# Optimization experiments

Measured on AMD Instinct MI355X. Metric: run time of the kernel, lower is better.

The kernel has to match this reference:

```python
import jax, jax.numpy as jnp
import numpy as np

REGION = 70  # region_width == region_height == receptive_field


def _localize(score_map, img_h, score_h):
    # stride=1, window=1x1 -> region_score is just the channel-mean at each pixel.
    B, _, Hs, Ws = score_map.shape
    m = score_map.mean(axis=1).reshape(B, -1)  # [B, Hs*Ws], row-major over (dim2, dim3)
    # loop order (i outer over dim2, j inner over dim3) + strict-inequality updates
    # == first-occurrence argmax/argmin in row-major order.
    imax = jnp.argmax(m, axis=1)
    vmax = jnp.max(m, axis=1)
    imin = jnp.argmin(m, axis=1)
    vmin = jnp.min(m, axis=1)
    rx = (imax // Ws).astype(jnp.float32)
    ry = (imax % Ws).astype(jnp.float32)
    fx = (imin // Ws).astype(jnp.float32)
    fy = (imin % Ws).astype(jnp.float32)
    # ax_tmp_real initialized to zeros (update iff score > 0); ax_tmp_fake to ones (iff score < 1)
    ax_real = jnp.where(vmax[:, None] > 0.0, jnp.stack([rx, ry], axis=1), 0.0)
    ax_fake = jnp.where(vmin[:, None] < 1.0, jnp.stack([fx, fy], axis=1), 1.0)
    img_stride = float((img_h - 70.0) // score_h)  # static python floor-div as in torch
    ax_real = ax_real * img_stride + 70.0
    ax_fake = ax_fake * img_stride + 70.0
    return ax_fake, ax_real


def _crop_one(img, row0, col0):
    # Faithful crop_and_resize (transform_fpcoor=True, crop size == box size == 70):
    # sample positions are row0 + [0..69], col0 + [0..69]; bilinear; zeros outside image.
    C, H, W = img.shape
    ys = row0 + jnp.arange(REGION, dtype=jnp.float32)
    xs = col0 + jnp.arange(REGION, dtype=jnp.float32)
    vy = (ys >= 0.0) & (ys <= H - 1.0)
    vx = (xs >= 0.0) & (xs <= W - 1.0)
    y0 = jnp.floor(ys)
    x0 = jnp.floor(xs)
    ly = ys - y0
    lx = xs - x0
    y0i = jnp.clip(y0.astype(jnp.int32), 0, H - 1)
    y1i = jnp.clip(y0i + 1, 0, H - 1)
    x0i = jnp.clip(x0.astype(jnp.int32), 0, W - 1)
    x1i = jnp.clip(x0i + 1, 0, W - 1)

    def gat(yi, xi):  # -> [C, 70, 70]
        return img[:, yi[:, None], xi[None, :]]

    top = gat(y0i, x0i) * (1.0 - lx)[None, None, :] + gat(y0i, x1i) * lx[None, None, :]
    bot = gat(y1i, x0i) * (1.0 - lx)[None, None, :] + gat(y1i, x1i) * lx[None, None, :]
    out = top * (1.0 - ly)[None, :, None] + bot * ly[None, :, None]
    mask = (vy[:, None] & vx[None, :]).astype(img.dtype)
    return out * mask[None]


_crop = jax.vmap(_crop_one)  # over batch


def _forward(real_B, fake_B, real_A, score_map):
    ax_fake, ax_real = _localize(score_map, real_B.shape[2], score_map.shape[2])
    ax_fake = jax.lax.stop_gradient(ax_fake)  # torch detaches via .cpu().numpy()
    ax_real = jax.lax.stop_gradient(ax_real)
    # boxes = [y, x, y+70, x+70] fed to RoIAlign as (x1,y1,x2,y2):
    # crop row start = ax[:,0] (the loop's _x, dim-2 index), col start = ax[:,1].
    fake_Bf = _crop(fake_B, ax_fake[:, 0], ax_fake[:, 1])
    real_Af = _crop(real_A, ax_fake[:, 0], ax_fake[:, 1])
    fake_ABf = jnp.concatenate((real_Af, fake_Bf), axis=1)
    fake_Br = _crop(fake_B, ax_real[:, 0], ax_real[:, 1])
    real_Ar = _crop(real_A, ax_real[:, 0], ax_real[:, 1])
    real_ABr = jnp.concatenate((real_Ar, fake_Br), axis=1)
    return (fake_Br, real_Ar, fake_Bf, real_Af, fake_ABf, real_ABr)


def setup_inputs() -> dict:
    key = jax.random.key(0)
    k1, k2, k3, k4 = jax.random.split(key, 4)
    B, H = 32, 512
    return {
        "real_B": jax.random.normal(k1, (B, 3, H, H), dtype=jnp.float32),
        "fake_B": jax.random.normal(k2, (B, 3, H, H), dtype=jnp.float32),
        "real_A": jax.random.normal(k3, (B, 3, H, H), dtype=jnp.float32),
        "score_map": jax.random.uniform(k4, (B, 1, 128, 128), dtype=jnp.float32),
    }


def reference(real_B, fake_B, real_A, score_map):
    return _forward(real_B, fake_B, real_A, score_map)
```

## Files before the change

kernel.cpp:

```cpp
#include <hip/hip_runtime.h>

#define SSZ   16384
#define SW    128
#define IMG   512
#define NPER  470400
#define OFF_AB_F 1881600
#define OFF_AB_R 2822400
#define CHUNKS 32
#define NF4_BATCH 14700
#define F4_PER_CHUNK 460

typedef float f4v __attribute__((ext_vector_type(4)));

__global__ __launch_bounds__(256)
void fused_crop_kernel(const float* __restrict__ fake_B,
                       const float* __restrict__ real_A,
                       const float* __restrict__ score,
                       float* __restrict__ out) {
    const int blk   = blockIdx.x;
    const int b     = blk >> 5;
    const int chunk = blk & 31;
    const int t     = threadIdx.x;

    const float4* s4 = (const float4*)(score + (size_t)b * SSZ);
    float vmax = -__builtin_inff(); int imax = 0;
    float vmin =  __builtin_inff(); int imin = 0;
    #pragma unroll
    for (int it = 0; it < 16; ++it) {
        const int q = it * 256 + t;
        const float4 v = s4[q];
        const int e = q * 4;
        if (v.x > vmax) { vmax = v.x; imax = e;     }
        if (v.y > vmax) { vmax = v.y; imax = e + 1; }
        if (v.z > vmax) { vmax = v.z; imax = e + 2; }
        if (v.w > vmax) { vmax = v.w; imax = e + 3; }
        if (v.x < vmin) { vmin = v.x; imin = e;     }
        if (v.y < vmin) { vmin = v.y; imin = e + 1; }
        if (v.z < vmin) { vmin = v.z; imin = e + 2; }
        if (v.w < vmin) { vmin = v.w; imin = e + 3; }
    }
    #pragma unroll
    for (int off = 1; off < 64; off <<= 1) {
        const float mv = __shfl_xor(vmax, off); const int mi = __shfl_xor(imax, off);
        if (mv > vmax || (mv == vmax && mi < imax)) { vmax = mv; imax = mi; }
        const float nv = __shfl_xor(vmin, off); const int ni = __shfl_xor(imin, off);
        if (nv < vmin || (nv == vmin && ni < imin)) { vmin = nv; imin = ni; }
    }
    __shared__ float sv[8];
    __shared__ int   si[8];
    if ((t & 63) == 0) {
        const int w = t >> 6;
        sv[w] = vmax; si[w] = imax;
        sv[w + 4] = vmin; si[w + 4] = imin;
    }
    __syncthreads();
    float bmax = sv[0]; int bimax = si[0];
    float bmin = sv[4]; int bimin = si[4];
    #pragma unroll
    for (int w = 1; w < 4; ++w) {
        if (sv[w] > bmax || (sv[w] == bmax && si[w] < bimax)) { bmax = sv[w]; bimax = si[w]; }
        if (sv[w+4] < bmin || (sv[w+4] == bmin && si[w+4] < bimin)) { bmin = sv[w+4]; bimin = si[w+4]; }
    }
    int rr, rc, fr, fc;
    if (bmax > 0.0f) { rr = bimax / SW; rc = bimax % SW; } else { rr = 0; rc = 0; }
    if (bmin < 1.0f) { fr = bimin / SW; fc = bimin % SW; } else { fr = 1; fc = 1; }
    const int row0r = rr * 3 + 70, col0r = rc * 3 + 70;
    const int row0f = fr * 3 + 70, col0f = fc * 3 + 70;

    const size_t srcb = (size_t)b * 3 * (IMG * IMG);
    const int e0 = chunk * F4_PER_CHUNK;
    const int e1 = min(e0 + F4_PER_CHUNK, NF4_BATCH);
    for (int e = e0 + t; e < e1; e += 256) {
        const int k    = e / 3675;
        const int rem  = e - k * 3675;
        const int c    = rem / 1225;
        const int f4   = rem - c * 1225;
        const int flat = f4 * 4;
        const int i0   = flat / 70;
        const int j0   = flat - i0 * 70;

        const int row0 = (k < 2) ? row0r : row0f;
        const int col0 = (k < 2) ? col0r : col0f;
        const float* src = (k == 0 || k == 2) ? fake_B : real_A;
        const float* sp  = src + srcb + (size_t)c * (IMG * IMG);

        f4v v;
        #pragma unroll
        for (int s = 0; s < 4; ++s) {
            int i = i0, j = j0 + s;
            if (j >= 70) { j -= 70; ++i; }
            const int y = row0 + i, x = col0 + j;
            v[s] = (y < IMG && x < IMG) ? sp[y * IMG + x] : 0.0f;
        }

        const size_t inner = (size_t)c * 4900 + flat;
        const size_t prim  = (size_t)k * NPER + (size_t)b * 14700 + inner;
        const size_t cb    = ((k < 2) ? (size_t)OFF_AB_R : (size_t)OFF_AB_F)
                             + (size_t)b * 29400
                             + ((k & 1) ? 0 : 3) * 4900
                             + inner;
        __builtin_nontemporal_store(v, (f4v*)(out + prim));
        __builtin_nontemporal_store(v, (f4v*)(out + cb));
    }
}

extern "C" void kernel_launch(void* const* d_in, const int* in_sizes, int n_in,
                              void* d_out, int out_size, void* d_ws, size_t ws_size,
                              hipStream_t stream) {
    const float* fake_B    = (const float*)d_in[1];
    const float* real_A    = (const float*)d_in[2];
    const float* score_map = (const float*)d_in[3];
    float* out = (float*)d_out;

    fused_crop_kernel<<<32 * CHUNKS, 256, 0, stream>>>(fake_B, real_A, score_map, out);
}
```

Before: 18.11 us.

## Split localization into separate partial-reduction kernel and double crop chunk count

Before, each of the 32 crop blocks per batch re-read the whole 64KB score map to find argmax/argmin. Now a small kernel reduces 16 slices per batch into packed sortable 64-bit keys in workspace. The crop kernel merges those 32 keys and runs on twice as many smaller chunks. This removes the redundant score reads, but adds a second kernel launch and a dependency between the two kernels.

```diff
diff --git a/kernel.cpp b/kernel.cpp
--- a/kernel.cpp
+++ b/kernel.cpp
@@ -6,30 +6,31 @@
 #define NPER  470400
 #define OFF_AB_F 1881600
 #define OFF_AB_R 2822400
-#define CHUNKS 32
 #define NF4_BATCH 14700
-#define F4_PER_CHUNK 460
+#define CHUNKS 64
+#define F4_PER_CHUNK 230
 
 typedef float f4v __attribute__((ext_vector_type(4)));
+typedef unsigned long long u64;
 
-__global__ __launch_bounds__(256)
-void fused_crop_kernel(const float* __restrict__ fake_B,
-                       const float* __restrict__ real_A,
-                       const float* __restrict__ score,
-                       float* __restrict__ out) {
-    const int blk   = blockIdx.x;
-    const int b     = blk >> 5;
-    const int chunk = blk & 31;
-    const int t     = threadIdx.x;
+__device__ __forceinline__ unsigned ord_f32(float v) {
+    unsigned s = __float_as_uint(v);
+    return (s & 0x80000000u) ? ~s : (s | 0x80000000u);
+}
 
-    const float4* s4 = (const float4*)(score + (size_t)b * SSZ);
+__global__ __launch_bounds__(64)
+void localize_partial(const float* __restrict__ score, u64* __restrict__ keys) {
+    const int blk = blockIdx.x;
+    const int b = blk >> 4, sl = blk & 15;
+    const int t = threadIdx.x;
+    const float4* p4 = (const float4*)(score + (size_t)b * SSZ + sl * 1024);
+
     float vmax = -__builtin_inff(); int imax = 0;
     float vmin =  __builtin_inff(); int imin = 0;
     #pragma unroll
-    for (int it = 0; it < 16; ++it) {
-        const int q = it * 256 + t;
-        const float4 v = s4[q];
-        const int e = q * 4;
+    for (int q = 0; q < 4; ++q) {
+        const float4 v = p4[t + 64 * q];
+        const int e = sl * 1024 + (t + 64 * q) * 4;
         if (v.x > vmax) { vmax = v.x; imax = e;     }
         if (v.y > vmax) { vmax = v.y; imax = e + 1; }
         if (v.z > vmax) { vmax = v.z; imax = e + 2; }
@@ -46,21 +47,36 @@
         const float nv = __shfl_xor(vmin, off); const int ni = __shfl_xor(imin, off);
         if (nv < vmin || (nv == vmin && ni < imin)) { vmin = nv; imin = ni; }
     }
-    __shared__ float sv[8];
-    __shared__ int   si[8];
-    if ((t & 63) == 0) {
-        const int w = t >> 6;
-        sv[w] = vmax; si[w] = imax;
-        sv[w + 4] = vmin; si[w + 4] = imin;
+    if (t == 0) {
+        keys[b * 32 + sl]      = ((u64)ord_f32(vmax) << 32) | (unsigned)~imax;
+        keys[b * 32 + 16 + sl] = ((u64)ord_f32(vmin) << 32) | (unsigned)imin;
     }
-    __syncthreads();
-    float bmax = sv[0]; int bimax = si[0];
-    float bmin = sv[4]; int bimin = si[4];
+}
+
+__global__ __launch_bounds__(256)
+void crop_kernel(const float* __restrict__ fake_B,
+                 const float* __restrict__ real_A,
+                 const u64* __restrict__ keys,
+                 float* __restrict__ out) {
+    const int blk   = blockIdx.x;
+    const int b     = blk / CHUNKS;
+    const int chunk = blk % CHUNKS;
+    const int t     = threadIdx.x;
+
+    const u64* kb = keys + b * 32;
+    u64 km = kb[0], kn = kb[16];
     #pragma unroll
-    for (int w = 1; w < 4; ++w) {
-        if (sv[w] > bmax || (sv[w] == bmax && si[w] < bimax)) { bmax = sv[w]; bimax = si[w]; }
-        if (sv[w+4] < bmin || (sv[w+4] == bmin && si[w+4] < bimin)) { bmin = sv[w+4]; bimin = si[w+4]; }
+    for (int s = 1; s < 16; ++s) {
+        const u64 a = kb[s];      if (a > km) km = a;
+        const u64 c = kb[16 + s]; if (c < kn) kn = c;
     }
+    const unsigned uh = (unsigned)(km >> 32);
+    const float bmax = __uint_as_float((uh & 0x80000000u) ? (uh & 0x7FFFFFFFu) : ~uh);
+    const int bimax = (int)~(unsigned)km;
+    const unsigned un = (unsigned)(kn >> 32);
+    const float bmin = __uint_as_float((un & 0x80000000u) ? (un & 0x7FFFFFFFu) : ~un);
+    const int bimin = (int)(unsigned)kn;
+
     int rr, rc, fr, fc;
     if (bmax > 0.0f) { rr = bimax / SW; rc = bimax % SW; } else { rr = 0; rc = 0; }
     if (bmin < 1.0f) { fr = bimin / SW; fc = bimin % SW; } else { fr = 1; fc = 1; }
@@ -81,9 +97,8 @@
 
         const int row0 = (k < 2) ? row0r : row0f;
         const int col0 = (k < 2) ? col0r : col0f;
-        const float* src = (k == 0 || k == 2) ? fake_B : real_A;
-        const float* sp  = src + srcb + (size_t)c * (IMG * IMG);
-
+        const float* sp = ((k == 0 || k == 2) ? fake_B : real_A)
+                          + srcb + (size_t)c * (IMG * IMG);
         f4v v;
         #pragma unroll
         for (int s = 0; s < 4; ++s) {
@@ -111,6 +126,8 @@
     const float* real_A    = (const float*)d_in[2];
     const float* score_map = (const float*)d_in[3];
     float* out = (float*)d_out;
+    u64*   keys = (u64*)d_ws;
 
-    fused_crop_kernel<<<32 * CHUNKS, 256, 0, stream>>>(fake_B, real_A, score_map, out);
+    localize_partial<<<32 * 16, 64, 0, stream>>>(score_map, keys);
+    crop_kernel<<<32 * CHUNKS, 256, 0, stream>>>(fake_B, real_A, keys, out);
 }
```

After: 15.93 us. -12.1%, faster.

## Use fewer larger blocks, vectorized unaligned row loads, and plain stores

Applied to the files above, without the earlier changes.

Changes the launch from 1024 blocks of 256 threads to 256 blocks of 1024 threads, so each batch's score argmax/argmin is recomputed 8 times instead of 32. The gather now uses a single unaligned 4-wide load when the four elements lie in one row and inside the image, and falls back to scalar loads otherwise. Nontemporal output stores are replaced with ordinary vector stores. The trade-off is fewer blocks across the CUs (256 blocks, below the GPU's CU count) and a larger per-block reduction.

```diff
diff --git a/kernel.cpp b/kernel.cpp
--- a/kernel.cpp
+++ b/kernel.cpp
@@ -6,30 +6,29 @@
 #define NPER  470400
 #define OFF_AB_F 1881600
 #define OFF_AB_R 2822400
-#define CHUNKS 32
 #define NF4_BATCH 14700
-#define F4_PER_CHUNK 460
+#define BPB   8
+#define F4_PER_BLK 1838
 
-typedef float f4v __attribute__((ext_vector_type(4)));
+typedef float f4v   __attribute__((ext_vector_type(4)));
+typedef float f4v_u __attribute__((ext_vector_type(4), aligned(4)));
 
-__global__ __launch_bounds__(256)
-void fused_crop_kernel(const float* __restrict__ fake_B,
-                       const float* __restrict__ real_A,
-                       const float* __restrict__ score,
-                       float* __restrict__ out) {
-    const int blk   = blockIdx.x;
-    const int b     = blk >> 5;
-    const int chunk = blk & 31;
+__global__ __launch_bounds__(1024)
+void fused_all(const float* __restrict__ fake_B,
+               const float* __restrict__ real_A,
+               const float* __restrict__ score,
+               float* __restrict__ out) {
+    const int b     = blockIdx.x >> 3;
+    const int chunk = blockIdx.x & 7;
     const int t     = threadIdx.x;
 
-    const float4* s4 = (const float4*)(score + (size_t)b * SSZ);
+    const float4* p4 = (const float4*)(score + (size_t)b * SSZ);
     float vmax = -__builtin_inff(); int imax = 0;
     float vmin =  __builtin_inff(); int imin = 0;
     #pragma unroll
-    for (int it = 0; it < 16; ++it) {
-        const int q = it * 256 + t;
-        const float4 v = s4[q];
-        const int e = q * 4;
+    for (int q = 0; q < 4; ++q) {
+        const float4 v = p4[t + 1024 * q];
+        const int e = (t + 1024 * q) * 4;
         if (v.x > vmax) { vmax = v.x; imax = e;     }
         if (v.y > vmax) { vmax = v.y; imax = e + 1; }
         if (v.z > vmax) { vmax = v.z; imax = e + 2; }
@@ -46,31 +45,31 @@
         const float nv = __shfl_xor(vmin, off); const int ni = __shfl_xor(imin, off);
         if (nv < vmin || (nv == vmin && ni < imin)) { vmin = nv; imin = ni; }
     }
-    __shared__ float sv[8];
-    __shared__ int   si[8];
+    __shared__ float sv[32];
+    __shared__ int   si[32];
+    const int w = t >> 6;
     if ((t & 63) == 0) {
-        const int w = t >> 6;
-        sv[w] = vmax; si[w] = imax;
-        sv[w + 4] = vmin; si[w + 4] = imin;
+        sv[w]      = vmax; si[w]      = imax;
+        sv[w + 16] = vmin; si[w + 16] = imin;
     }
     __syncthreads();
-    float bmax = sv[0]; int bimax = si[0];
-    float bmin = sv[4]; int bimin = si[4];
+    float bm = sv[0];  int bi = si[0];
+    float nm = sv[16]; int ni = si[16];
     #pragma unroll
-    for (int w = 1; w < 4; ++w) {
-        if (sv[w] > bmax || (sv[w] == bmax && si[w] < bimax)) { bmax = sv[w]; bimax = si[w]; }
-        if (sv[w+4] < bmin || (sv[w+4] == bmin && si[w+4] < bimin)) { bmin = sv[w+4]; bimin = si[w+4]; }
+    for (int x = 1; x < 16; ++x) {
+        if (sv[x] > bm || (sv[x] == bm && si[x] < bi)) { bm = sv[x]; bi = si[x]; }
+        if (sv[x+16] < nm || (sv[x+16] == nm && si[x+16] < ni)) { nm = sv[x+16]; ni = si[x+16]; }
     }
     int rr, rc, fr, fc;
-    if (bmax > 0.0f) { rr = bimax / SW; rc = bimax % SW; } else { rr = 0; rc = 0; }
-    if (bmin < 1.0f) { fr = bimin / SW; fc = bimin % SW; } else { fr = 1; fc = 1; }
+    if (bm > 0.0f) { rr = bi / SW; rc = bi % SW; } else { rr = 0; rc = 0; }
+    if (nm < 1.0f) { fr = ni / SW; fc = ni % SW; } else { fr = 1; fc = 1; }
     const int row0r = rr * 3 + 70, col0r = rc * 3 + 70;
     const int row0f = fr * 3 + 70, col0f = fc * 3 + 70;
 
     const size_t srcb = (size_t)b * 3 * (IMG * IMG);
-    const int e0 = chunk * F4_PER_CHUNK;
-    const int e1 = min(e0 + F4_PER_CHUNK, NF4_BATCH);
-    for (int e = e0 + t; e < e1; e += 256) {
+    const int e0 = chunk * F4_PER_BLK;
+    const int e1 = min(e0 + F4_PER_BLK, NF4_BATCH);
+    for (int e = e0 + t; e < e1; e += 1024) {
         const int k    = e / 3675;
         const int rem  = e - k * 3675;
         const int c    = rem / 1225;
@@ -81,16 +80,22 @@
 
         const int row0 = (k < 2) ? row0r : row0f;
         const int col0 = (k < 2) ? col0r : col0f;
-        const float* src = (k == 0 || k == 2) ? fake_B : real_A;
-        const float* sp  = src + srcb + (size_t)c * (IMG * IMG);
+        const float* sp = ((k == 0 || k == 2) ? fake_B : real_A)
+                          + srcb + (size_t)c * (IMG * IMG);
+        const int y = row0 + i0;
+        const int x = col0 + j0;
 
         f4v v;
-        #pragma unroll
-        for (int s = 0; s < 4; ++s) {
-            int i = i0, j = j0 + s;
-            if (j >= 70) { j -= 70; ++i; }
-            const int y = row0 + i, x = col0 + j;
-            v[s] = (y < IMG && x < IMG) ? sp[y * IMG + x] : 0.0f;
+        if (j0 != 68 && y < IMG && x + 3 < IMG) {
+            v = *(const f4v_u*)(sp + y * IMG + x);
+        } else {
+            #pragma unroll
+            for (int s = 0; s < 4; ++s) {
+                int i = i0, j = j0 + s;
+                if (j >= 70) { j -= 70; ++i; }
+                const int yy = row0 + i, xx = col0 + j;
+                v[s] = (yy < IMG && xx < IMG) ? sp[yy * IMG + xx] : 0.0f;
+            }
         }
 
         const size_t inner = (size_t)c * 4900 + flat;
@@ -99,8 +104,8 @@
                              + (size_t)b * 29400
                              + ((k & 1) ? 0 : 3) * 4900
                              + inner;
-        __builtin_nontemporal_store(v, (f4v*)(out + prim));
-        __builtin_nontemporal_store(v, (f4v*)(out + cb));
+        *(f4v*)(out + prim) = v;
+        *(f4v*)(out + cb)   = v;
     }
 }
 
@@ -112,5 +117,5 @@
     const float* score_map = (const float*)d_in[3];
     float* out = (float*)d_out;
 
-    fused_crop_kernel<<<32 * CHUNKS, 256, 0, stream>>>(fake_B, real_A, score_map, out);
+    fused_all<<<32 * BPB, 1024, 0, stream>>>(fake_B, real_A, score_map, out);
 }
```

New measurement: 16.36 us. -9.7%, faster.
